# Optimization experiments

Measured on AMD Instinct MI355X. Metric: run time of the kernel, lower is better.

Reference implementation:

```python
import jax, jax.numpy as jnp
import numpy as np

B, S, V, E, H, T = 128, 512, 6000, 100, 256, 9


def setup_inputs() -> dict:
    key = jax.random.key(0)
    ks = jax.random.split(key, 16)
    lengths = jax.random.randint(ks[0], (B,), S // 4, S + 1)
    mask = (jnp.arange(S)[None, :] < lengths[:, None])  # [B,S] bool, contiguous prefixes
    data = jax.random.randint(ks[1], (B, S), 1, V)
    data = jnp.where(mask, data, 0)  # pad token = 0 (padding_idx)
    sc = 0.1
    emb = jax.random.normal(ks[2], (V, E), jnp.float32) * sc
    emb = emb.at[0].set(0.0)  # padding_idx=0
    return {
        "data": data, "mask": mask,
        "emb": emb,
        "W_ih_f": jax.random.normal(ks[3], (4 * H, E), jnp.float32) * sc,
        "W_hh_f": jax.random.normal(ks[4], (4 * H, H), jnp.float32) * sc,
        "b_f": jax.random.normal(ks[5], (4 * H,), jnp.float32) * sc,
        "W_ih_b": jax.random.normal(ks[6], (4 * H, E), jnp.float32) * sc,
        "W_hh_b": jax.random.normal(ks[7], (4 * H, H), jnp.float32) * sc,
        "b_b": jax.random.normal(ks[8], (4 * H,), jnp.float32) * sc,
        "mlp_W": jax.random.normal(ks[9], (T, 2 * H), jnp.float32) * sc,
        "mlp_b": jax.random.normal(ks[10], (T,), jnp.float32) * sc,
        "start_trans": jax.random.normal(ks[11], (T,), jnp.float32) * sc,
        "trans": jax.random.normal(ks[12], (T, T), jnp.float32) * sc,
        "end_trans": jax.random.normal(ks[13], (T,), jnp.float32) * sc,
    }


def _lstm_dir(xg, W_hh, reverse):
    # xg: [S,B,4H] precomputed input projection + biases
    h0 = jnp.zeros((xg.shape[1], W_hh.shape[1]), xg.dtype)

    def step(carry, xt):
        h, c = carry
        g = xt + h @ W_hh.T
        i, f, gg, o = jnp.split(g, 4, axis=-1)  # PyTorch gate order i,f,g,o
        c = jax.nn.sigmoid(f) * c + jax.nn.sigmoid(i) * jnp.tanh(gg)
        h = jax.nn.sigmoid(o) * jnp.tanh(c)
        return (h, c), h

    _, hs = jax.lax.scan(step, (h0, h0), xg, reverse=reverse)
    return hs  # [S,B,H]


def _emissions(data, emb, W_ih_f, W_hh_f, b_f, W_ih_b, W_hh_b, b_b, mlp_W, mlp_b):
    x = emb[data]  # [B,S,E]
    xg_f = jnp.einsum('bse,ge->sbg', x, W_ih_f) + b_f
    xg_b = jnp.einsum('bse,ge->sbg', x, W_ih_b) + b_b
    hf = _lstm_dir(xg_f, W_hh_f, False)
    hb = _lstm_dir(xg_b, W_hh_b, True)
    h = jnp.concatenate([hf, hb], axis=-1)  # [S,B,2H]
    return jnp.einsum('sbh,th->bst', h, mlp_W) + mlp_b  # [B,S,T]


def _viterbi(em, mask, start_trans, trans, end_trans):
    b, s, t = em.shape
    score0 = start_trans + em[:, 0]  # [B,T]
    em_t = jnp.swapaxes(em, 0, 1)[1:]      # [S-1,B,T]
    mask_t = jnp.swapaxes(mask, 0, 1)[1:]  # [S-1,B]

    def step(score, inp):
        e_t, m_t = inp
        cand = score[:, :, None] + trans[None] + e_t[:, None, :]  # [B,Tprev,Tcur]
        new = cand.max(axis=1)
        bp = cand.argmax(axis=1).astype(jnp.int32)  # [B,T]
        score = jnp.where(m_t[:, None], new, score)
        return score, bp

    score, bps = jax.lax.scan(step, score0, (em_t, mask_t))
    final = score + end_trans
    best_score = final.max(axis=-1)               # [B]
    last_tag = final.argmax(axis=-1).astype(jnp.int32)

    def back(tag, inp):
        bp, m_t = inp
        prev = jnp.take_along_axis(bp, tag[:, None], axis=1)[:, 0]
        prev = jnp.where(m_t, prev, tag)
        return prev, tag

    first_tag, tags_rest = jax.lax.scan(back, last_tag, (bps, mask_t), reverse=True)
    paths = jnp.concatenate([first_tag[None], tags_rest], axis=0)  # [S,B]
    paths = jnp.where(jnp.swapaxes(mask, 0, 1), paths, 0)
    return jnp.swapaxes(paths, 0, 1), best_score


def reference(data, mask, emb, W_ih_f, W_hh_f, b_f, W_ih_b, W_hh_b, b_b,
              mlp_W, mlp_b, start_trans, trans, end_trans):
    em = _emissions(data, emb, W_ih_f, W_hh_f, b_f, W_ih_b, W_hh_b, b_b, mlp_W, mlp_b)
    paths, best_score = _viterbi(em, mask, start_trans, trans, end_trans)
    return paths, best_score
```

## Files before the change

kernel.cpp:

```cpp
#include <hip/hip_runtime.h>
#include <math.h>
#include <stdint.h>

#define B 128
#define S 512
#define V 6000
#define E 100
#define H 256
#define G4 1024
#define T 9

#define WREG 20
#define WLDS 3
#define WSTR 41

#define OFF_PEMB_F 0u
#define PEMB_BYTES (V*G4*4u)
#define OFF_PEMB_B (OFF_PEMB_F + PEMB_BYTES)
#define OFF_EMF    (OFF_PEMB_B + PEMB_BYTES)
#define EM_BYTES   (B*S*T*4u)
#define OFF_EMB    (OFF_EMF + EM_BYTES)
#define OFF_BP     (OFF_EMB + EM_BYTES)
#define BP_BYTES   ((S-1)*B*16u)
#define OFF_LT     (OFF_BP + BP_BYTES)
#define OFF_PT     (OFF_LT + 512u)
#define OFF_WSTREAM OFF_BP

__device__ __forceinline__ float sigf(float x) { return 1.0f / (1.0f + expf(-x)); }

__global__ __launch_bounds__(256) void k_pemb(const float* __restrict__ emb,
                                              const float* __restrict__ wf, const float* __restrict__ bf,
                                              const float* __restrict__ wb, const float* __restrict__ bb,
                                              char* __restrict__ ws) {
    int blk = blockIdx.x;
    int d   = blk >= 375;
    int vb  = d ? blk - 375 : blk;
    const float* W    = d ? wb : wf;
    const float* bias = d ? bb : bf;
    float* pe = (float*)(ws + (d ? OFF_PEMB_B : OFF_PEMB_F));

    __shared__ float es[16 * E];
    for (int i = threadIdx.x; i < 16 * E; i += 256) es[i] = emb[vb * 16 * E + i];
    __syncthreads();

    int j = threadIdx.x;
    float acc[4][16];
    #pragma unroll
    for (int q = 0; q < 4; q++) {
        float bq = bias[q * H + j];
        #pragma unroll
        for (int v = 0; v < 16; v++) acc[q][v] = bq;
    }
    for (int e = 0; e < E; e++) {
        float w0 = W[(0 * H + j) * E + e];
        float w1 = W[(1 * H + j) * E + e];
        float w2 = W[(2 * H + j) * E + e];
        float w3 = W[(3 * H + j) * E + e];
        #pragma unroll
        for (int v = 0; v < 16; v++) {
            float x = es[v * E + e];
            acc[0][v] += w0 * x; acc[1][v] += w1 * x;
            acc[2][v] += w2 * x; acc[3][v] += w3 * x;
        }
    }
    for (int v = 0; v < 16; v++)
        #pragma unroll
        for (int q = 0; q < 4; q++)
            pe[(vb * 16 + v) * G4 + q * H + j] = acc[q][v];
}

__global__ __launch_bounds__(256) void k_prep(const float* __restrict__ whhf,
                                              const float* __restrict__ whhb,
                                              char* __restrict__ ws) {
    int tid = blockIdx.x * 256 + threadIdx.x;
    if (tid >= 2 * WSTR * 1024) return;
    int d   = tid >= WSTR * 1024;
    int idx = d ? tid - WSTR * 1024 : tid;
    int g = idx >> 10, r = idx & 1023;
    const float* whh = d ? whhb : whhf;
    float4* wstr = (float4*)(ws + OFF_WSTREAM);
    const float4* src = (const float4*)(whh + (size_t)r * H + 4 * (WREG + WLDS));
    wstr[((size_t)(d * WSTR + g) << 10) + r] = src[g];
}

__global__ __attribute__((amdgpu_flat_work_group_size(512, 512), amdgpu_waves_per_eu(2, 2)))
void k_lstm(const int* __restrict__ data,
            const float* __restrict__ whhf,
            const float* __restrict__ whhb,
            const float* __restrict__ mlpW,
            char* __restrict__ ws) {
    int blk = blockIdx.x;
    int d = blk >> 7, b = blk & 127;
    const float* whh = d ? whhb : whhf;
    const float* pe  = (const float*)(ws + (d ? OFF_PEMB_B : OFF_PEMB_F));
    float* emdst = (float*)(ws + (d ? OFF_EMB : OFF_EMF));
    const float4* wstr = (const float4*)(ws + OFF_WSTREAM) + ((size_t)(d * WSTR) << 10);

    __shared__ __align__(16) float hs[H];
    __shared__ float4 sW[WLDS << 10];
    __shared__ float  gbuf[G4];
    __shared__ int    toks[S];

    int t = threadIdx.x;
    int r0 = t, r1 = t + 512;

    const float4* wrow0 = (const float4*)(whh + (size_t)r0 * H);
    const float4* wrow1 = (const float4*)(whh + (size_t)r1 * H);
    float4 wA[WREG], wB[WREG];
    #pragma unroll
    for (int g = 0; g < WREG; g++) { wA[g] = wrow0[g]; wB[g] = wrow1[g]; }
    #pragma unroll
    for (int g = 0; g < WREG; g++) {
        asm volatile("" : "+v"(wA[g].x), "+v"(wA[g].y), "+v"(wA[g].z), "+v"(wA[g].w));
        asm volatile("" : "+v"(wB[g].x), "+v"(wB[g].y), "+v"(wB[g].z), "+v"(wB[g].w));
    }
    #pragma unroll
    for (int g = 0; g < WLDS; g++) {
        sW[(g << 10) + r0] = wrow0[WREG + g];
        sW[(g << 10) + r1] = wrow1[WREG + g];
    }

    toks[t] = data[b * S + t];

    float mwE[16];
    int tt = (t - 256) >> 4, el = (t - 256) & 15;
    if (t >= 256 && t < 256 + 16 * T) {
        #pragma unroll
        for (int k = 0; k < 16; k++)
            mwE[k] = mlpW[tt * (2 * H) + d * H + el + 16 * k];
    }
    if (t < H) hs[t] = 0.0f;
    float cst = 0.0f;
    __syncthreads();

    const float4* hs4 = (const float4*)hs;
    const float4* wsp0 = wstr + r0;
    const float4* wsp1 = wstr + r1;

    float pf0, pf1;
    {
        int sp0 = d ? (S - 1) : 0;
        size_t tok = (size_t)toks[sp0];
        pf0 = pe[(tok << 10) + r0];
        pf1 = pe[(tok << 10) + r1];
    }

    for (int ss = 0; ss < S; ss++) {
        int sp = d ? (S - 1 - ss) : ss;
        float acc0 = pf0, acc1 = pf1;
        if (ss + 1 < S) {
            int spn = d ? (S - 2 - ss) : (ss + 1);
            size_t tok = (size_t)toks[spn];
            pf0 = pe[(tok << 10) + r0];
            pf1 = pe[(tok << 10) + r1];
        }

        #pragma unroll
        for (int g = 0; g < WREG; g++) {
            float4 h4 = hs4[g];
            float4 a = wA[g], bb2 = wB[g];
            acc0 = fmaf(a.x, h4.x, acc0);  acc1 = fmaf(bb2.x, h4.x, acc1);
            acc0 = fmaf(a.y, h4.y, acc0);  acc1 = fmaf(bb2.y, h4.y, acc1);
            acc0 = fmaf(a.z, h4.z, acc0);  acc1 = fmaf(bb2.z, h4.z, acc1);
            acc0 = fmaf(a.w, h4.w, acc0);  acc1 = fmaf(bb2.w, h4.w, acc1);
        }
        #pragma unroll
        for (int g = 0; g < WLDS; g++) {
            float4 w0 = sW[(g << 10) + r0];
            float4 w1 = sW[(g << 10) + r1];
            float4 h4 = hs4[WREG + g];
            acc0 = fmaf(w0.x, h4.x, acc0);  acc1 = fmaf(w1.x, h4.x, acc1);
            acc0 = fmaf(w0.y, h4.y, acc0);  acc1 = fmaf(w1.y, h4.y, acc1);
            acc0 = fmaf(w0.z, h4.z, acc0);  acc1 = fmaf(w1.z, h4.z, acc1);
            acc0 = fmaf(w0.w, h4.w, acc0);  acc1 = fmaf(w1.w, h4.w, acc1);
        }
        #pragma unroll 4
        for (int g = 0; g < WSTR; g++) {
            float4 w0 = wsp0[(size_t)g << 10];
            float4 w1 = wsp1[(size_t)g << 10];
            float4 h4 = hs4[WREG + WLDS + g];
            acc0 = fmaf(w0.x, h4.x, acc0);  acc1 = fmaf(w1.x, h4.x, acc1);
            acc0 = fmaf(w0.y, h4.y, acc0);  acc1 = fmaf(w1.y, h4.y, acc1);
            acc0 = fmaf(w0.z, h4.z, acc0);  acc1 = fmaf(w1.z, h4.z, acc1);
            acc0 = fmaf(w0.w, h4.w, acc0);  acc1 = fmaf(w1.w, h4.w, acc1);
        }
        gbuf[r0] = acc0;
        gbuf[r1] = acc1;
        __syncthreads();

        if (t < 256) {
            float gi = gbuf[t], gf = gbuf[H + t], gg = gbuf[2 * H + t], go = gbuf[3 * H + t];
            float ig = sigf(gi), fg = sigf(gf), tg = tanhf(gg), og = sigf(go);
            cst = fg * cst + ig * tg;
            float hn = og * tanhf(cst);
            hs[t] = hn;
        }
        __syncthreads();

        if (t >= 256 && t < 256 + 16 * T) {
            float v = 0.0f;
            #pragma unroll
            for (int k = 0; k < 16; k++) v = fmaf(hs[el + 16 * k], mwE[k], v);
            v += __shfl_xor(v, 8, 16);
            v += __shfl_xor(v, 4, 16);
            v += __shfl_xor(v, 2, 16);
            v += __shfl_xor(v, 1, 16);
            if (el == 0)
                emdst[((size_t)b * S + sp) * T + tt] = v;
        }
    }
}

__global__ __launch_bounds__(64) void k_vit(const int* __restrict__ data,
                                            const float* __restrict__ strans,
                                            const float* __restrict__ trans,
                                            const float* __restrict__ etrans,
                                            const float* __restrict__ mlpb,
                                            float* __restrict__ out,
                                            char* __restrict__ ws) {
    int b = blockIdx.x, t = threadIdx.x;
    const float* emf = (const float*)(ws + OFF_EMF);
    const float* emb = (const float*)(ws + OFF_EMB);
    char* bp = ws + OFF_BP;
    int*  lt = (int*)(ws + OFF_LT);
    bool act = t < T;

    float trp[T];
    float mb = 0.0f;
    if (act) {
        #pragma unroll
        for (int p = 0; p < T; p++) trp[p] = trans[p * T + t];
        mb = mlpb[t];
    }
    float score = -1e30f;
    if (act) score = strans[t] + emf[(b * S) * T + t] + emb[(b * S) * T + t] + mb;

    for (int s = 1; s < S; s++) {
        float e = 0.0f;
        if (act) e = emf[(b * S + s) * T + t] + emb[(b * S + s) * T + t] + mb;
        float best = __shfl(score, 0, 64) + trp[0];
        int bpi = 0;
        #pragma unroll
        for (int p = 1; p < T; p++) {
            float cand = __shfl(score, p, 64) + trp[p];
            if (cand > best) { best = cand; bpi = p; }
        }
        int m = data[b * S + s] != 0;
        if (act) {
            score = m ? (best + e) : score;
            bp[((size_t)(s - 1) * B + b) * 16 + t] = (char)bpi;
        }
    }
    float fin = act ? score + etrans[t] : -1e30f;
    float bv = __shfl(fin, 0, 64);
    int bi = 0;
    #pragma unroll
    for (int p = 1; p < T; p++) {
        float v = __shfl(fin, p, 64);
        if (v > bv) { bv = v; bi = p; }
    }
    if (t == 0) { out[B * S + b] = bv; lt[b] = bi; }
}

__global__ __launch_bounds__(128) void k_back(const int* __restrict__ data, char* __restrict__ ws) {
    int b = threadIdx.x;
    const int4* bp4 = (const int4*)(ws + OFF_BP);
    const int*  lt  = (const int*)(ws + OFF_LT);
    int* pt = (int*)(ws + OFF_PT);
    int tag = lt[b];
    pt[(S - 1) * B + b] = tag;
    for (int p = S - 2; p >= 0; p--) {
        int4 r = bp4[(size_t)p * B + b];
        int m = data[b * S + p + 1] != 0;
        unsigned w = (unsigned)(tag < 8 ? (tag < 4 ? r.x : r.y) : r.z);
        int nt = (int)((w >> ((tag & 3) * 8)) & 0xff);
        tag = m ? nt : tag;
        pt[p * B + b] = tag;
    }
}

__global__ __launch_bounds__(256) void k_fin(const int* __restrict__ data,
                                             float* __restrict__ out,
                                             const char* __restrict__ ws) {
    int tid = blockIdx.x * 256 + threadIdx.x;
    const int* pt = (const int*)(ws + OFF_PT);
    int b = tid >> 9, p = tid & 511;
    out[tid] = (data[tid] != 0) ? (float)pt[p * B + b] : 0.0f;
}

extern "C" void kernel_launch(void* const* d_in, const int* in_sizes, int n_in,
                              void* d_out, int out_size, void* d_ws, size_t ws_size,
                              hipStream_t stream) {
    const int*   data = (const int*)d_in[0];
    const float* emb  = (const float*)d_in[2];
    const float* wihf = (const float*)d_in[3];
    const float* whhf = (const float*)d_in[4];
    const float* bf   = (const float*)d_in[5];
    const float* wihb = (const float*)d_in[6];
    const float* whhb = (const float*)d_in[7];
    const float* bb   = (const float*)d_in[8];
    const float* mlpW = (const float*)d_in[9];
    const float* mlpb = (const float*)d_in[10];
    const float* st   = (const float*)d_in[11];
    const float* tr   = (const float*)d_in[12];
    const float* et   = (const float*)d_in[13];
    float* out = (float*)d_out;
    char*  ws  = (char*)d_ws;

    hipLaunchKernelGGL(k_pemb, dim3(750),  dim3(256), 0, stream, emb, wihf, bf, wihb, bb, ws);
    hipLaunchKernelGGL(k_prep, dim3(328),  dim3(256), 0, stream, whhf, whhb, ws);
    hipLaunchKernelGGL(k_lstm, dim3(256),  dim3(512), 0, stream, data, whhf, whhb, mlpW, ws);
    hipLaunchKernelGGL(k_vit,  dim3(128),  dim3(64),  0, stream, data, st, tr, et, mlpb, out, ws);
    hipLaunchKernelGGL(k_back, dim3(1),    dim3(128), 0, stream, data, ws);
    hipLaunchKernelGGL(k_fin,  dim3(256),  dim3(256), 0, stream, data, out, ws);
}
```

Measured before the change: 4.167 ms.

## Pair LSTM blocks over two batch rows, split hidden units across workgroups

Replaces the per-sequence LSTM kernel with one where each pair of workgroups jointly processes two batch rows, each workgroup owning half of the hidden units. The halves of h are exchanged every timestep through global memory using release/acquire flags, and the matvec is split so the local-half work overlaps the wait for the partner. This halves the weight work per row per block and reuses each weight load for two batch rows, at the cost of a cross-workgroup spin-wait per step that depends on both blocks being co-resident. The new path runs only when the workspace is large enough; otherwise it falls back to the old kernel.

Result: slower. 9.161 ms (+119.9%).

```diff
diff --git a/kernel.cpp b/kernel.cpp
--- a/kernel.cpp
+++ b/kernel.cpp
@@ -25,6 +25,11 @@
 #define OFF_LT     (OFF_BP + BP_BYTES)
 #define OFF_PT     (OFF_LT + 512u)
 #define OFF_WSTREAM OFF_BP
+#define OFF_HX  (OFF_BP + 1343488u)
+#define HX_BYTES (2u*128u*2u*2u*128u*4u)
+#define OFF_FLG (OFF_HX + HX_BYTES)
+#define FLG_BYTES (256u*4u)
+#define WS_NEED ((size_t)OFF_FLG + FLG_BYTES)
 
 __device__ __forceinline__ float sigf(float x) { return 1.0f / (1.0f + expf(-x)); }
 
@@ -81,6 +86,237 @@
     float4* wstr = (float4*)(ws + OFF_WSTREAM);
     const float4* src = (const float4*)(whh + (size_t)r * H + 4 * (WREG + WLDS));
     wstr[((size_t)(d * WSTR + g) << 10) + r] = src[g];
+}
+
+__global__ __launch_bounds__(256) void k_zflg(char* __restrict__ ws) {
+    ((int*)(ws + OFF_FLG))[threadIdx.x] = 0;
+}
+
+__global__ __attribute__((amdgpu_flat_work_group_size(512, 512), amdgpu_waves_per_eu(2, 2)))
+void k_lstm2(const int* __restrict__ data,
+             const float* __restrict__ whhf,
+             const float* __restrict__ whhb,
+             const float* __restrict__ mlpW,
+             char* __restrict__ ws) {
+    int blk = blockIdx.x;
+    int q = blk >> 7, job = blk & 127;
+    int d = job >> 6, p = job & 63;
+    int b0 = 2 * p, b1 = b0 + 1;
+    const float* whh = d ? whhb : whhf;
+    const float* pe  = (const float*)(ws + (d ? OFF_PEMB_B : OFF_PEMB_F));
+    float* emdst = (float*)(ws + (d ? OFF_EMB : OFF_EMF));
+    const float4* wstr = (const float4*)(ws + OFF_WSTREAM) + ((size_t)(d * WSTR) << 10);
+    float* hxf = (float*)(ws + OFF_HX);
+    int* flg = (int*)(ws + OFF_FLG);
+    int* flg_self = flg + job * 2 + q;
+    int* flg_part = flg + job * 2 + (1 - q);
+
+    __shared__ __align__(16) float hs[2][H];
+    __shared__ float4 sW[WLDS << 9];
+    __shared__ float  gbuf[2 * 512];
+    __shared__ int    toks[2][S];
+
+    int t = threadIdx.x;
+    int gq = t >> 7, uo = t & 127;
+    int row = gq * 256 + q * 128 + uo;
+    int oth = 1 - q;
+
+    const float4* wrow = (const float4*)(whh + (size_t)row * H);
+    float4 wP[WREG];
+    #pragma unroll
+    for (int g = 0; g < WREG; g++) wP[g] = wrow[g];
+    #pragma unroll
+    for (int g = 0; g < WREG; g++)
+        asm volatile("" : "+v"(wP[g].x), "+v"(wP[g].y), "+v"(wP[g].z), "+v"(wP[g].w));
+
+    #pragma unroll
+    for (int j = 0; j < WLDS; j++) sW[(j << 9) + t] = wrow[WREG + j];
+
+    toks[0][t] = data[b0 * S + t];
+    toks[1][t] = data[b1 * S + t];
+
+    float mwE[16];
+    int ebi = t / 144, erem = t - ebi * 144, ett = erem >> 4, eel = erem & 15;
+    if (q == 0 && t < 288) {
+        #pragma unroll
+        for (int k = 0; k < 16; k++)
+            mwE[k] = mlpW[ett * (2 * H) + d * H + eel + 16 * k];
+    }
+    if (t < 256) { hs[0][t] = 0.0f; hs[1][t] = 0.0f; }
+    float cst = 0.0f;
+    __syncthreads();
+
+    const float4* h40 = (const float4*)&hs[0][0];
+    const float4* h41 = (const float4*)&hs[1][0];
+    const float4* wsp = wstr + row;
+
+    float pf0, pf1;
+    {
+        int sp0 = d ? (S - 1) : 0;
+        pf0 = pe[((size_t)toks[0][sp0] << 10) + row];
+        pf1 = pe[((size_t)toks[1][sp0] << 10) + row];
+    }
+
+    int spPrev = 0;
+    for (int ss = 0; ss < S; ss++) {
+        int sp = d ? (S - 1 - ss) : ss;
+        float a0 = pf0, a1 = pf1;
+        if (ss + 1 < S) {
+            int spn = d ? (S - 2 - ss) : (ss + 1);
+            pf0 = pe[((size_t)toks[0][spn] << 10) + row];
+            pf1 = pe[((size_t)toks[1][spn] << 10) + row];
+        }
+
+        if (q == 0) {
+            #pragma unroll
+            for (int g = 0; g < WREG; g++) {
+                float4 h0 = h40[g], h1 = h41[g], w = wP[g];
+                a0 = fmaf(w.x, h0.x, a0);  a1 = fmaf(w.x, h1.x, a1);
+                a0 = fmaf(w.y, h0.y, a0);  a1 = fmaf(w.y, h1.y, a1);
+                a0 = fmaf(w.z, h0.z, a0);  a1 = fmaf(w.z, h1.z, a1);
+                a0 = fmaf(w.w, h0.w, a0);  a1 = fmaf(w.w, h1.w, a1);
+            }
+            #pragma unroll
+            for (int j = 0; j < WLDS; j++) {
+                float4 h0 = h40[WREG + j], h1 = h41[WREG + j], w = sW[(j << 9) + t];
+                a0 = fmaf(w.x, h0.x, a0);  a1 = fmaf(w.x, h1.x, a1);
+                a0 = fmaf(w.y, h0.y, a0);  a1 = fmaf(w.y, h1.y, a1);
+                a0 = fmaf(w.z, h0.z, a0);  a1 = fmaf(w.z, h1.z, a1);
+                a0 = fmaf(w.w, h0.w, a0);  a1 = fmaf(w.w, h1.w, a1);
+            }
+            #pragma unroll 3
+            for (int s2 = 0; s2 < 9; s2++) {
+                float4 w = wsp[(size_t)s2 << 10];
+                float4 h0 = h40[23 + s2], h1 = h41[23 + s2];
+                a0 = fmaf(w.x, h0.x, a0);  a1 = fmaf(w.x, h1.x, a1);
+                a0 = fmaf(w.y, h0.y, a0);  a1 = fmaf(w.y, h1.y, a1);
+                a0 = fmaf(w.z, h0.z, a0);  a1 = fmaf(w.z, h1.z, a1);
+                a0 = fmaf(w.w, h0.w, a0);  a1 = fmaf(w.w, h1.w, a1);
+            }
+        } else {
+            #pragma unroll 4
+            for (int s2 = 9; s2 < 41; s2++) {
+                float4 w = wsp[(size_t)s2 << 10];
+                float4 h0 = h40[23 + s2], h1 = h41[23 + s2];
+                a0 = fmaf(w.x, h0.x, a0);  a1 = fmaf(w.x, h1.x, a1);
+                a0 = fmaf(w.y, h0.y, a0);  a1 = fmaf(w.y, h1.y, a1);
+                a0 = fmaf(w.z, h0.z, a0);  a1 = fmaf(w.z, h1.z, a1);
+                a0 = fmaf(w.w, h0.w, a0);  a1 = fmaf(w.w, h1.w, a1);
+            }
+        }
+
+        if (ss > 0) {
+            if (t == 0) {
+                while (__hip_atomic_load(flg_part, __ATOMIC_ACQUIRE,
+                                         __HIP_MEMORY_SCOPE_AGENT) < ss)
+                    __builtin_amdgcn_s_sleep(1);
+            }
+            __syncthreads();
+            if (t < 256) {
+                int bi = t >> 7, u2 = t & 127;
+                int idx = ((((((ss - 1) & 1) * 128 + job) * 2 + oth) * 2 + bi) << 7) + u2;
+                hs[bi][oth * 128 + u2] =
+                    __hip_atomic_load(hxf + idx, __ATOMIC_RELAXED, __HIP_MEMORY_SCOPE_AGENT);
+            }
+            __syncthreads();
+            if (q == 0 && t < 288) {
+                float v = 0.0f;
+                #pragma unroll
+                for (int k = 0; k < 16; k++) v = fmaf(hs[ebi][eel + 16 * k], mwE[k], v);
+                v += __shfl_xor(v, 8, 16);
+                v += __shfl_xor(v, 4, 16);
+                v += __shfl_xor(v, 2, 16);
+                v += __shfl_xor(v, 1, 16);
+                if (eel == 0)
+                    emdst[((size_t)(b0 + ebi) * S + spPrev) * T + ett] = v;
+            }
+        }
+
+        if (q == 0) {
+            #pragma unroll 4
+            for (int s2 = 9; s2 < 41; s2++) {
+                float4 w = wsp[(size_t)s2 << 10];
+                float4 h0 = h40[23 + s2], h1 = h41[23 + s2];
+                a0 = fmaf(w.x, h0.x, a0);  a1 = fmaf(w.x, h1.x, a1);
+                a0 = fmaf(w.y, h0.y, a0);  a1 = fmaf(w.y, h1.y, a1);
+                a0 = fmaf(w.z, h0.z, a0);  a1 = fmaf(w.z, h1.z, a1);
+                a0 = fmaf(w.w, h0.w, a0);  a1 = fmaf(w.w, h1.w, a1);
+            }
+        } else {
+            #pragma unroll
+            for (int g = 0; g < WREG; g++) {
+                float4 h0 = h40[g], h1 = h41[g], w = wP[g];
+                a0 = fmaf(w.x, h0.x, a0);  a1 = fmaf(w.x, h1.x, a1);
+                a0 = fmaf(w.y, h0.y, a0);  a1 = fmaf(w.y, h1.y, a1);
+                a0 = fmaf(w.z, h0.z, a0);  a1 = fmaf(w.z, h1.z, a1);
+                a0 = fmaf(w.w, h0.w, a0);  a1 = fmaf(w.w, h1.w, a1);
+            }
+            #pragma unroll
+            for (int j = 0; j < WLDS; j++) {
+                float4 h0 = h40[WREG + j], h1 = h41[WREG + j], w = sW[(j << 9) + t];
+                a0 = fmaf(w.x, h0.x, a0);  a1 = fmaf(w.x, h1.x, a1);
+                a0 = fmaf(w.y, h0.y, a0);  a1 = fmaf(w.y, h1.y, a1);
+                a0 = fmaf(w.z, h0.z, a0);  a1 = fmaf(w.z, h1.z, a1);
+                a0 = fmaf(w.w, h0.w, a0);  a1 = fmaf(w.w, h1.w, a1);
+            }
+            #pragma unroll 3
+            for (int s2 = 0; s2 < 9; s2++) {
+                float4 w = wsp[(size_t)s2 << 10];
+                float4 h0 = h40[23 + s2], h1 = h41[23 + s2];
+                a0 = fmaf(w.x, h0.x, a0);  a1 = fmaf(w.x, h1.x, a1);
+                a0 = fmaf(w.y, h0.y, a0);  a1 = fmaf(w.y, h1.y, a1);
+                a0 = fmaf(w.z, h0.z, a0);  a1 = fmaf(w.z, h1.z, a1);
+                a0 = fmaf(w.w, h0.w, a0);  a1 = fmaf(w.w, h1.w, a1);
+            }
+        }
+
+        gbuf[t] = a0;
+        gbuf[512 + t] = a1;
+        __syncthreads();
+
+        if (t < 256) {
+            int bi = t >> 7, u2 = t & 127;
+            float gi = gbuf[bi * 512 + u2],       gf = gbuf[bi * 512 + 128 + u2];
+            float gg = gbuf[bi * 512 + 256 + u2], go = gbuf[bi * 512 + 384 + u2];
+            float ig = sigf(gi), fg = sigf(gf), tg = tanhf(gg), og = sigf(go);
+            cst = fg * cst + ig * tg;
+            float hn = og * tanhf(cst);
+            hs[bi][q * 128 + u2] = hn;
+            int idx = (((((ss & 1) * 128 + job) * 2 + q) * 2 + bi) << 7) + u2;
+            __hip_atomic_store(hxf + idx, hn, __ATOMIC_RELAXED, __HIP_MEMORY_SCOPE_AGENT);
+        }
+        __syncthreads();
+        if (t == 0) {
+            __threadfence();
+            __hip_atomic_store(flg_self, ss + 1, __ATOMIC_RELEASE, __HIP_MEMORY_SCOPE_AGENT);
+        }
+        spPrev = sp;
+    }
+
+    if (t == 0) {
+        while (__hip_atomic_load(flg_part, __ATOMIC_ACQUIRE,
+                                 __HIP_MEMORY_SCOPE_AGENT) < S)
+            __builtin_amdgcn_s_sleep(1);
+    }
+    __syncthreads();
+    if (t < 256) {
+        int bi = t >> 7, u2 = t & 127;
+        int idx = ((((((S - 1) & 1) * 128 + job) * 2 + oth) * 2 + bi) << 7) + u2;
+        hs[bi][oth * 128 + u2] =
+            __hip_atomic_load(hxf + idx, __ATOMIC_RELAXED, __HIP_MEMORY_SCOPE_AGENT);
+    }
+    __syncthreads();
+    if (q == 0 && t < 288) {
+        float v = 0.0f;
+        #pragma unroll
+        for (int k = 0; k < 16; k++) v = fmaf(hs[ebi][eel + 16 * k], mwE[k], v);
+        v += __shfl_xor(v, 8, 16);
+        v += __shfl_xor(v, 4, 16);
+        v += __shfl_xor(v, 2, 16);
+        v += __shfl_xor(v, 1, 16);
+        if (eel == 0)
+            emdst[((size_t)(b0 + ebi) * S + spPrev) * T + ett] = v;
+    }
 }
 
 __global__ __attribute__((amdgpu_flat_work_group_size(512, 512), amdgpu_waves_per_eu(2, 2)))
@@ -307,9 +543,16 @@
     float* out = (float*)d_out;
     char*  ws  = (char*)d_ws;
 
+    int pair_ok = (ws_size >= WS_NEED);
+
     hipLaunchKernelGGL(k_pemb, dim3(750),  dim3(256), 0, stream, emb, wihf, bf, wihb, bb, ws);
     hipLaunchKernelGGL(k_prep, dim3(328),  dim3(256), 0, stream, whhf, whhb, ws);
-    hipLaunchKernelGGL(k_lstm, dim3(256),  dim3(512), 0, stream, data, whhf, whhb, mlpW, ws);
+    if (pair_ok) {
+        hipLaunchKernelGGL(k_zflg,  dim3(1),   dim3(256), 0, stream, ws);
+        hipLaunchKernelGGL(k_lstm2, dim3(256), dim3(512), 0, stream, data, whhf, whhb, mlpW, ws);
+    } else {
+        hipLaunchKernelGGL(k_lstm,  dim3(256), dim3(512), 0, stream, data, whhf, whhb, mlpW, ws);
+    }
     hipLaunchKernelGGL(k_vit,  dim3(128),  dim3(64),  0, stream, data, st, tr, et, mlpb, out, ws);
     hipLaunchKernelGGL(k_back, dim3(1),    dim3(128), 0, stream, data, ws);
     hipLaunchKernelGGL(k_fin,  dim3(256),  dim3(256), 0, stream, data, out, ws);
```
